# Performance work log

Hardware: AMD Instinct MI355X
Metric: run time of the kernel (lower is better)

Reference implementation:

```python
import jax, jax.numpy as jnp
import numpy as np

B, L, D = 4, 4096, 1024
K = D // 4

def setup_inputs() -> dict:
    key = jax.random.key(0)
    ks = jax.random.split(key, 16)
    def w(k, sh):
        return jax.random.normal(k, sh, dtype=jnp.float32) * 0.02
    return {
        'x': jax.random.normal(ks[0], (B, L, D), dtype=jnp.float32),
        'Wk1': w(ks[1], (D, D)), 'bk1': jnp.zeros((D,), jnp.float32),
        'Wk2': w(ks[2], (D, K * 4)), 'bk2': jnp.zeros((K * 4,), jnp.float32),
        'Wq1': w(ks[3], (D, D)), 'bq1': jnp.zeros((D,), jnp.float32),
        'Wq2': w(ks[4], (D, K * 4)), 'bq2': jnp.zeros((K * 4,), jnp.float32),
        'Wv': w(ks[5], (D, D)), 'bv': jnp.zeros((D,), jnp.float32),
        'gamma': jnp.ones((D,), jnp.float32), 'beta': jnp.zeros((D,), jnp.float32),
        'Wo': w(ks[6], (D, D)), 'bo': jnp.zeros((D,), jnp.float32),
    }

def _normalize(q, eps=1e-12):
    n = jnp.sqrt(jnp.sum(q * q, axis=-1, keepdims=True))
    return q / jnp.maximum(n, eps)

def _quat_conj(q):
    return q * jnp.asarray([1., -1., -1., -1.], dtype=q.dtype)

def _quat_mul(q1, q2):
    w1, x1, y1, z1 = q1[..., 0], q1[..., 1], q1[..., 2], q1[..., 3]
    w2, x2, y2, z2 = q2[..., 0], q2[..., 1], q2[..., 2], q2[..., 3]
    w = w1 * w2 - x1 * x2 - y1 * y2 - z1 * z2
    x = w1 * x2 + x1 * w2 + y1 * z2 - z1 * y2
    y = w1 * y2 - x1 * z2 + y1 * w2 + z1 * x2
    z = w1 * z2 + x1 * y2 - y1 * x2 + z1 * w2
    return jnp.stack([w, x, y, z], axis=-1)

def _quat_rotate(q, v):
    return _quat_mul(_quat_mul(q, v), _quat_conj(q))

def _mlp(x, W1, b1, W2, b2):
    h = jax.nn.gelu(x @ W1 + b1, approximate=False)
    return h @ W2 + b2

def _layernorm(x, g, b, eps=1e-5):
    mu = jnp.mean(x, axis=-1, keepdims=True)
    var = jnp.var(x, axis=-1, keepdims=True)
    return (x - mu) * jax.lax.rsqrt(var + eps) * g + b

def reference(x, Wk1, bk1, Wk2, bk2, Wq1, bq1, Wq2, bq2, Wv, bv, gamma, beta, Wo, bo):
    b, l, d = x.shape
    k = d // 4
    key_q = _normalize(_mlp(x, Wk1, bk1, Wk2, bk2).reshape(b, l, k, 4))
    query_q = _normalize(_mlp(x, Wq1, bq1, Wq2, bq2).reshape(b, l, k, 4))
    value = (x @ Wv + bv).reshape(b, l, k, 4)
    rotated = _quat_rotate(key_q, value)            # [B,L,K,4]
    memory = jnp.cumsum(rotated, axis=1)            # prefix-sum memory
    retrieved = _quat_rotate(_quat_conj(query_q), memory).reshape(b, l, d)
    norm = jnp.sqrt(jnp.arange(1, l + 1, dtype=x.dtype)).reshape(1, l, 1)
    out = _layernorm(retrieved / norm, gamma, beta) @ Wo + bo
    return x + out
```

## Files before the change

### kernel.cpp

```cpp
#include <hip/hip_runtime.h>
#include <cstddef>
#include <cstdint>

static constexpr int Bb  = 4;
static constexpr int Ll  = 4096;
static constexpr int Dd  = 1024;
static constexpr int Mm  = 16384;
static constexpr int KK  = 1024;
static constexpr int NTK = 32;

typedef __attribute__((ext_vector_type(8))) short short8;
typedef __attribute__((ext_vector_type(4))) float f32x4;

#define AS1C(p) ((const __attribute__((address_space(1))) void*)(p))
#define AS3(p)  ((__attribute__((address_space(3))) void*)(p))

__device__ __forceinline__ float b2f(unsigned short u) {
    union { unsigned int i; float f; } c; c.i = ((unsigned int)u) << 16; return c.f;
}
__device__ __forceinline__ unsigned short f2b(float f) {
    union { float f; unsigned int i; } c; c.f = f;
    unsigned int r = c.i + 0x7fffu + ((c.i >> 16) & 1u);
    return (unsigned short)(r >> 16);
}
__device__ __forceinline__ float4 qmul(const float4 a, const float4 b) {
    float4 r;
    r.x = a.x * b.x - a.y * b.y - a.z * b.z - a.w * b.w;
    r.y = a.x * b.y + a.y * b.x + a.z * b.w - a.w * b.z;
    r.z = a.x * b.z - a.y * b.w + a.z * b.x + a.w * b.y;
    r.w = a.x * b.w + a.y * b.z - a.z * b.y + a.w * b.x;
    return r;
}
__device__ __forceinline__ float4 qconj(const float4 a) {
    return make_float4(a.x, -a.y, -a.z, -a.w);
}
__device__ __forceinline__ float4 qnorm(const float4 a) {
    float n = sqrtf(a.x * a.x + a.y * a.y + a.z * a.z + a.w * a.w);
    float inv = 1.0f / fmaxf(n, 1e-12f);
    return make_float4(a.x * inv, a.y * inv, a.z * inv, a.w * inv);
}
__device__ __forceinline__ float gelu_fast(float v) {
    const float a = fabsf(v) * 0.70710678118654752f;
    const float t = 1.0f / (1.0f + 0.3275911f * a);
    const float p = t * (0.254829592f + t * (-0.284496736f + t * (1.421413741f
                   + t * (-1.453152027f + t * 1.061405429f))));
    const float e = __expf(-a * a);
    const float erfa = 1.0f - p * e;
    const float erfv = copysignf(erfa, v);
    return 0.5f * v * (1.0f + erfv);
}

__global__ __launch_bounds__(256)
void conv_k(const float* __restrict__ src, unsigned short* __restrict__ dst, int n4)
{
    const int i = blockIdx.x * 256 + threadIdx.x;
    if (i >= n4) return;
    const float4 v = reinterpret_cast<const float4*>(src)[i];
    ushort4 o;
    o.x = f2b(v.x); o.y = f2b(v.y); o.z = f2b(v.z); o.w = f2b(v.w);
    reinterpret_cast<ushort4*>(dst)[i] = o;
}

__global__ __launch_bounds__(256)
void wtrans_k(const float* __restrict__ src, unsigned short* __restrict__ dst)
{
    __shared__ float t[32][33];
    const int tx = threadIdx.x, ty = threadIdx.y;
    const int n0 = blockIdx.x * 32, k0 = blockIdx.y * 32;
    #pragma unroll
    for (int j = ty; j < 32; j += 8)
        t[j][tx] = src[(size_t)(k0 + j) * Dd + n0 + tx];
    __syncthreads();
    #pragma unroll
    for (int j = ty; j < 32; j += 8)
        dst[(size_t)(n0 + j) * Dd + k0 + tx] = f2b(t[tx][j]);
}

__global__ __launch_bounds__(256)
void bcat_k(const float* __restrict__ bk1, const float* __restrict__ bq1,
            const float* __restrict__ bv,  const float* __restrict__ bk2,
            const float* __restrict__ bq2, float* __restrict__ b1,
            float* __restrict__ b2)
{
    const int i = blockIdx.x * 256 + threadIdx.x;
    if (i < 3072) b1[i] = (i < 1024) ? bk1[i] : (i < 2048 ? bq1[i - 1024] : bv[i - 2048]);
    if (i < 2048) b2[i] = (i < 1024) ? bk2[i] : bq2[i - 1024];
}

template<int MODE>
__global__ __launch_bounds__(512, 2)
void gemm256_k(const unsigned short* __restrict__ A, int astride,
               const unsigned short* __restrict__ BT,
               const float* __restrict__ bias,
               const float* __restrict__ resid,
               unsigned short* __restrict__ outH,
               float* __restrict__ outF,
               int Nn)
{
    extern __shared__ char smem[];
    const int tid  = threadIdx.x;
    const int lane = tid & 63;
    const int w    = tid >> 6;
    const int wr   = w >> 2;
    const int wc   = w & 3;

    const int nwg = gridDim.x;
    const int cpx = nwg >> 3;
    const int bid = blockIdx.x;
    const int swz = (bid & 7) * cpx + (bid >> 3);
    const int nTN = Nn >> 8;
    const int m0  = (swz / nTN) << 8;
    const int n0  = (swz % nTN) << 8;
    const int aoff = (MODE == 1 && n0 >= 1024) ? 1024 : 0;

    const unsigned short* gA[2];
    const unsigned short* gB[2];
    #pragma unroll
    for (int c = 0; c < 2; ++c) {
        const int n16 = c * 512 + tid;
        const int line = n16 >> 3;
        const int u = (n16 & 7) ^ (line & 7);
        const int r = 2 * line + (u >> 2);
        const int kcs = u & 3;
        gA[c] = A + (size_t)(m0 + r) * astride + aoff + kcs * 8;
        gB[c] = BT + (size_t)(n0 + r) * KK + kcs * 8;
    }
    const int wslot = w * 1024;

    auto STAGE = [&](int kt, int bi) {
        const int koff = kt * 32;
        #pragma unroll
        for (int c = 0; c < 2; ++c) {
            __builtin_amdgcn_global_load_lds(AS1C(gA[c] + koff),
                AS3(smem + bi * 16384 + c * 8192 + wslot), 16, 0, 0);
            __builtin_amdgcn_global_load_lds(AS1C(gB[c] + koff),
                AS3(smem + 49152 + bi * 16384 + c * 8192 + wslot), 16, 0, 0);
        }
    };

    const int kc = lane >> 4;
    const int rl = lane & 15;
    int offA[8], offB[4];
    #pragma unroll
    for (int mi = 0; mi < 8; ++mi) {
        const int r = wr * 128 + mi * 16 + rl;
        offA[mi] = (r >> 1) * 128 + (((((r & 1) << 2) | kc) ^ ((r >> 1) & 7)) << 4);
    }
    #pragma unroll
    for (int ni = 0; ni < 4; ++ni) {
        const int r = wc * 64 + ni * 16 + rl;
        offB[ni] = 49152 + (r >> 1) * 128 + (((((r & 1) << 2) | kc) ^ ((r >> 1) & 7)) << 4);
    }

    f32x4 acc[8][4] = {};

    auto BODY = [&](int kt, int bi, int bi2, int vm, bool dostage) {
        if (dostage) STAGE(kt + 2, bi2);
        const char* Ab = smem + bi * 16384;
        short8 af[4], bf[4];
        #pragma unroll
        for (int ni = 0; ni < 4; ++ni) bf[ni] = *(const short8*)(smem + bi * 16384 + offB[ni]);
        #pragma unroll
        for (int mi = 0; mi < 4; ++mi) af[mi] = *(const short8*)(Ab + offA[mi]);
        __builtin_amdgcn_s_barrier();
        __builtin_amdgcn_s_setprio(1);
        #pragma unroll
        for (int mi = 0; mi < 4; ++mi)
            #pragma unroll
            for (int ni = 0; ni < 4; ++ni)
                acc[mi][ni] = __builtin_amdgcn_mfma_f32_16x16x32_bf16(af[mi], bf[ni], acc[mi][ni], 0, 0, 0);
        __builtin_amdgcn_s_setprio(0);
        __builtin_amdgcn_s_barrier();
        #pragma unroll
        for (int mi = 0; mi < 4; ++mi) af[mi] = *(const short8*)(Ab + offA[4 + mi]);
        __builtin_amdgcn_s_setprio(1);
        #pragma unroll
        for (int mi = 0; mi < 4; ++mi)
            #pragma unroll
            for (int ni = 0; ni < 4; ++ni)
                acc[4 + mi][ni] = __builtin_amdgcn_mfma_f32_16x16x32_bf16(af[mi], bf[ni], acc[4 + mi][ni], 0, 0, 0);
        __builtin_amdgcn_s_setprio(0);
        if (vm == 4)      asm volatile("s_waitcnt vmcnt(4)" ::: "memory");
        else if (vm == 0) asm volatile("s_waitcnt vmcnt(0)" ::: "memory");
        if (vm >= 0) __builtin_amdgcn_s_barrier();
    };

    STAGE(0, 0);
    STAGE(1, 1);
    asm volatile("s_waitcnt vmcnt(4)" ::: "memory");
    __builtin_amdgcn_s_barrier();

    for (int t0 = 0; t0 < NTK - 2; t0 += 3) {
        BODY(t0 + 0, 0, 2, 4, true);
        BODY(t0 + 1, 1, 0, 4, true);
        BODY(t0 + 2, 2, 1, 4, true);
    }
    BODY(NTK - 2, 0, 0, 0, false);
    BODY(NTK - 1, 1, 0, -1, false);

    const int colb = n0 + wc * 64 + rl;
    const int rowb = m0 + wr * 128 + kc * 4;
    #pragma unroll
    for (int ni = 0; ni < 4; ++ni) {
        const int col = colb + ni * 16;
        const float bv = bias[col];
        #pragma unroll
        for (int mi = 0; mi < 8; ++mi) {
            const int row0 = rowb + mi * 16;
            #pragma unroll
            for (int rr = 0; rr < 4; ++rr) {
                float v = acc[mi][ni][rr] + bv;
                const int row = row0 + rr;
                if (MODE == 0) {
                    if (n0 < 2048) outH[(size_t)row * 2048 + col] = f2b(gelu_fast(v));
                    else           outF[(size_t)row * 1024 + (col - 2048)] = v;
                } else if (MODE == 1) {
                    outH[(size_t)row * 2048 + col] = f2b(v);
                } else {
                    const size_t ix = (size_t)row * 1024 + col;
                    outF[ix] = v + resid[ix];
                }
            }
        }
    }
}

__global__ __launch_bounds__(256)
void rotfuse_k(const unsigned short* __restrict__ qb2, float* __restrict__ val,
               float* __restrict__ part)
{
    const int idx = blockIdx.x * 256 + threadIdx.x;
    const int kq  = idx & 255;
    const int ch  = (idx >> 8) & 63;
    const int b   = idx >> 14;
    const int row0 = b * Ll + ch * 64;
    float4 s = make_float4(0.f, 0.f, 0.f, 0.f);
    for (int i = 0; i < 64; ++i) {
        const int row = row0 + i;
        const ushort4 qu = *reinterpret_cast<const ushort4*>(qb2 + (size_t)row * 2048 + kq * 4);
        const float4 q = qnorm(make_float4(b2f(qu.x), b2f(qu.y), b2f(qu.z), b2f(qu.w)));
        float4* vp = reinterpret_cast<float4*>(val + (size_t)row * 1024 + kq * 4);
        const float4 r = qmul(qmul(q, *vp), qconj(q));
        *vp = r;
        s.x += r.x; s.y += r.y; s.z += r.z; s.w += r.w;
    }
    *reinterpret_cast<float4*>(part + (size_t)idx * 4) = s;
}

__global__ __launch_bounds__(256)
void scan2_k(float* __restrict__ part)
{
    const int idx = blockIdx.x * 256 + threadIdx.x;
    const int kq = idx & 255, b = idx >> 8;
    float4 run = make_float4(0.f, 0.f, 0.f, 0.f);
    for (int c = 0; c < 64; ++c) {
        float4* p = reinterpret_cast<float4*>(part + (((size_t)(b * 64 + c)) * 256 + kq) * 4);
        const float4 t = *p;
        *p = run;
        run.x += t.x; run.y += t.y; run.z += t.z; run.w += t.w;
    }
}

__global__ __launch_bounds__(256)
void scan3_k(float* __restrict__ val, const float* __restrict__ part)
{
    const int idx = blockIdx.x * 256 + threadIdx.x;
    const int kq  = idx & 255;
    const int ch  = (idx >> 8) & 63;
    const int b   = idx >> 14;
    const int row0 = b * Ll + ch * 64;
    float4 run = *reinterpret_cast<const float4*>(part + (size_t)idx * 4);
    for (int i = 0; i < 64; ++i) {
        float4* vp = reinterpret_cast<float4*>(val + (size_t)(row0 + i) * 1024 + kq * 4);
        const float4 v = *vp;
        run.x += v.x; run.y += v.y; run.z += v.z; run.w += v.w;
        *vp = run;
    }
}

__global__ __launch_bounds__(256)
void retrieve_ln_k(const float* __restrict__ mem, const unsigned short* __restrict__ qb2,
                   const float* __restrict__ gamma, const float* __restrict__ beta,
                   unsigned short* __restrict__ out)
{
    const int row = blockIdx.x;
    const int l   = row & (Ll - 1);
    const int t   = threadIdx.x;
    const size_t base = (size_t)row * 1024 + t * 4;

    const ushort4 qu = *reinterpret_cast<const ushort4*>(qb2 + (size_t)row * 2048 + 1024 + t * 4);
    const float4 q = qnorm(make_float4(b2f(qu.x), b2f(qu.y), b2f(qu.z), b2f(qu.w)));
    const float4 m4 = *reinterpret_cast<const float4*>(mem + base);
    float4 r = qmul(qmul(qconj(q), m4), q);

    const float inv = 1.0f / sqrtf((float)(l + 1));
    r.x *= inv; r.y *= inv; r.z *= inv; r.w *= inv;

    float s  = r.x + r.y + r.z + r.w;
    float ss = r.x * r.x + r.y * r.y + r.z * r.z + r.w * r.w;
    #pragma unroll
    for (int off = 32; off > 0; off >>= 1) {
        s  += __shfl_xor(s, off);
        ss += __shfl_xor(ss, off);
    }
    __shared__ float red[2][4];
    const int wid = t >> 6, lane = t & 63;
    if (lane == 0) { red[0][wid] = s; red[1][wid] = ss; }
    __syncthreads();
    const float sum = red[0][0] + red[0][1] + red[0][2] + red[0][3];
    const float ssq = red[1][0] + red[1][1] + red[1][2] + red[1][3];
    const float mu  = sum * (1.0f / 1024.0f);
    const float var = ssq * (1.0f / 1024.0f) - mu * mu;
    const float sc  = rsqrtf(var + 1e-5f);

    const float4 g4 = *reinterpret_cast<const float4*>(gamma + t * 4);
    const float4 b4 = *reinterpret_cast<const float4*>(beta  + t * 4);
    ushort4 o;
    o.x = f2b((r.x - mu) * sc * g4.x + b4.x);
    o.y = f2b((r.y - mu) * sc * g4.y + b4.y);
    o.z = f2b((r.z - mu) * sc * g4.z + b4.z);
    o.w = f2b((r.w - mu) * sc * g4.w + b4.w);
    *reinterpret_cast<ushort4*>(out + base) = o;
}

extern "C" void kernel_launch(void* const* d_in, const int* in_sizes, int n_in,
                              void* d_out, int out_size, void* d_ws, size_t ws_size,
                              hipStream_t stream)
{
    const float* x     = (const float*)d_in[0];
    const float* Wk1   = (const float*)d_in[1];
    const float* bk1   = (const float*)d_in[2];
    const float* Wk2   = (const float*)d_in[3];
    const float* bk2   = (const float*)d_in[4];
    const float* Wq1   = (const float*)d_in[5];
    const float* bq1   = (const float*)d_in[6];
    const float* Wq2   = (const float*)d_in[7];
    const float* bq2   = (const float*)d_in[8];
    const float* Wv    = (const float*)d_in[9];
    const float* bv    = (const float*)d_in[10];
    const float* gamma = (const float*)d_in[11];
    const float* beta  = (const float*)d_in[12];
    const float* Wo    = (const float*)d_in[13];
    const float* bo    = (const float*)d_in[14];
    float* out = (float*)d_out;

    const size_t TD = (size_t)Mm * 1024;
    const size_t DD = (size_t)1024 * 1024;

    unsigned short* qb2   = (unsigned short*)d_ws;
    unsigned short* xb    = qb2;
    unsigned short* wcat1 = qb2 + TD;
    unsigned short* h     = qb2 + 2 * TD;
    float*          bufB  = (float*)(h + 2 * TD);
    unsigned short* wcat2 = (unsigned short*)(bufB + TD);
    unsigned short* woT   = wcat2 + 2 * DD;
    float*          bcat1 = (float*)(woT + DD);
    float*          bcat2 = bcat1 + 3072;
    float*          part  = bcat2 + 2048;

    const dim3 blk(256);
    const dim3 tblk(32, 8);
    const dim3 tgrid(32, 32);

    (void)hipFuncSetAttribute((const void*)gemm256_k<0>, hipFuncAttributeMaxDynamicSharedMemorySize, 98304);
    (void)hipFuncSetAttribute((const void*)gemm256_k<1>, hipFuncAttributeMaxDynamicSharedMemorySize, 98304);
    (void)hipFuncSetAttribute((const void*)gemm256_k<2>, hipFuncAttributeMaxDynamicSharedMemorySize, 98304);

    conv_k<<<(int)(TD / 4 / 256), blk, 0, stream>>>(x, xb, (int)(TD / 4));
    wtrans_k<<<tgrid, tblk, 0, stream>>>(Wk1, wcat1);
    wtrans_k<<<tgrid, tblk, 0, stream>>>(Wq1, wcat1 + DD);
    wtrans_k<<<tgrid, tblk, 0, stream>>>(Wv,  wcat1 + 2 * DD);
    wtrans_k<<<tgrid, tblk, 0, stream>>>(Wk2, wcat2);
    wtrans_k<<<tgrid, tblk, 0, stream>>>(Wq2, wcat2 + DD);
    wtrans_k<<<tgrid, tblk, 0, stream>>>(Wo,  woT);
    bcat_k<<<12, blk, 0, stream>>>(bk1, bq1, bv, bk2, bq2, bcat1, bcat2);

    gemm256_k<0><<<64 * 12, 512, 98304, stream>>>(xb, 1024, wcat1, bcat1, nullptr, h, bufB, 3072);
    gemm256_k<1><<<64 * 8, 512, 98304, stream>>>(h, 2048, wcat2, bcat2, nullptr, qb2, nullptr, 2048);

    rotfuse_k<<<256, blk, 0, stream>>>(qb2, bufB, part);
    scan2_k<<<4, blk, 0, stream>>>(part);
    scan3_k<<<256, blk, 0, stream>>>(bufB, part);

    retrieve_ln_k<<<Mm, blk, 0, stream>>>(bufB, qb2, gamma, beta, h);

    gemm256_k<2><<<64 * 4, 512, 98304, stream>>>(h, 1024, woT, bo, x, nullptr, out, 1024);
}
```

Measured before the change: 464.5 us.

## Restructure GEMM main loop into double-buffered 64-wide k phases; stage bf16 epilogue through LDS

The bf16 GEMM now uses two 64-deep k buffers (128 KB of LDS) instead of three 32-deep buffers. Each k-step is split into four phases, and each phase issues one unit of the next tile's global-to-LDS loads between its MFMA groups, so copies are interleaved more finely with compute. The bf16-output epilogues (GELU hidden and the second MLP) now write into LDS first, then store to global with 16-byte row-contiguous vector stores instead of scattered 2-byte stores. The cost is more LDS per block and extra barriers in the epilogue.

```diff
diff --git a/kernel.cpp b/kernel.cpp
--- a/kernel.cpp
+++ b/kernel.cpp
@@ -4,10 +4,9 @@
 
 static constexpr int Bb  = 4;
 static constexpr int Ll  = 4096;
-static constexpr int Dd  = 1024;
 static constexpr int Mm  = 16384;
 static constexpr int KK  = 1024;
-static constexpr int NTK = 32;
+static constexpr int NT2 = 16;
 
 typedef __attribute__((ext_vector_type(8))) short short8;
 typedef __attribute__((ext_vector_type(4))) float f32x4;
@@ -46,8 +45,7 @@
                    + t * (-1.453152027f + t * 1.061405429f))));
     const float e = __expf(-a * a);
     const float erfa = 1.0f - p * e;
-    const float erfv = copysignf(erfa, v);
-    return 0.5f * v * (1.0f + erfv);
+    return 0.5f * v * (1.0f + copysignf(erfa, v));
 }
 
 __global__ __launch_bounds__(256)
@@ -69,11 +67,11 @@
     const int n0 = blockIdx.x * 32, k0 = blockIdx.y * 32;
     #pragma unroll
     for (int j = ty; j < 32; j += 8)
-        t[j][tx] = src[(size_t)(k0 + j) * Dd + n0 + tx];
+        t[j][tx] = src[(size_t)(k0 + j) * 1024 + n0 + tx];
     __syncthreads();
     #pragma unroll
     for (int j = ty; j < 32; j += 8)
-        dst[(size_t)(n0 + j) * Dd + k0 + tx] = f2b(t[tx][j]);
+        dst[(size_t)(n0 + j) * 1024 + k0 + tx] = f2b(t[tx][j]);
 }
 
 __global__ __launch_bounds__(256)
@@ -113,28 +111,27 @@
     const int n0  = (swz % nTN) << 8;
     const int aoff = (MODE == 1 && n0 >= 1024) ? 1024 : 0;
 
-    const unsigned short* gA[2];
-    const unsigned short* gB[2];
-    #pragma unroll
-    for (int c = 0; c < 2; ++c) {
-        const int n16 = c * 512 + tid;
-        const int line = n16 >> 3;
-        const int u = (n16 & 7) ^ (line & 7);
-        const int r = 2 * line + (u >> 2);
-        const int kcs = u & 3;
-        gA[c] = A + (size_t)(m0 + r) * astride + aoff + kcs * 8;
-        gB[c] = BT + (size_t)(n0 + r) * KK + kcs * 8;
-    }
-    const int wslot = w * 1024;
-
-    auto STAGE = [&](int kt, int bi) {
-        const int koff = kt * 32;
+    const unsigned short* pA[2];
+    const unsigned short* pB[2];
+    #pragma unroll
+    for (int c2 = 0; c2 < 2; ++c2) {
+        const int s = c2 * 512 + tid;
+        const int line = s >> 3;
+        const int v = (s & 7) ^ (line & 7);
+        const int r = 2 * line + (v >> 2);
+        const int kcs = v & 3;
+        pA[c2] = A + (size_t)(m0 + r) * astride + aoff + kcs * 8;
+        pB[c2] = BT + (size_t)(n0 + r) * KK + kcs * 8;
+    }
+
+    auto STAGE_UNIT = [&](int cdst, int matB, int khs, int t1) {
+        const int ks = t1 * 64 + khs * 32;
         #pragma unroll
-        for (int c = 0; c < 2; ++c) {
-            __builtin_amdgcn_global_load_lds(AS1C(gA[c] + koff),
-                AS3(smem + bi * 16384 + c * 8192 + wslot), 16, 0, 0);
-            __builtin_amdgcn_global_load_lds(AS1C(gB[c] + koff),
-                AS3(smem + 49152 + bi * 16384 + c * 8192 + wslot), 16, 0, 0);
+        for (int c2 = 0; c2 < 2; ++c2) {
+            __builtin_amdgcn_global_load_lds(
+                AS1C((matB ? pB[c2] : pA[c2]) + ks),
+                AS3(smem + cdst * 65536 + matB * 32768 + khs * 16384 + c2 * 8192 + w * 1024),
+                16, 0, 0);
         }
     };
 
@@ -149,76 +146,105 @@
     #pragma unroll
     for (int ni = 0; ni < 4; ++ni) {
         const int r = wc * 64 + ni * 16 + rl;
-        offB[ni] = 49152 + (r >> 1) * 128 + (((((r & 1) << 2) | kc) ^ ((r >> 1) & 7)) << 4);
+        offB[ni] = 32768 + (r >> 1) * 128 + (((((r & 1) << 2) | kc) ^ ((r >> 1) & 7)) << 4);
     }
 
     f32x4 acc[8][4] = {};
-
-    auto BODY = [&](int kt, int bi, int bi2, int vm, bool dostage) {
-        if (dostage) STAGE(kt + 2, bi2);
-        const char* Ab = smem + bi * 16384;
-        short8 af[4], bf[4];
-        #pragma unroll
-        for (int ni = 0; ni < 4; ++ni) bf[ni] = *(const short8*)(smem + bi * 16384 + offB[ni]);
-        #pragma unroll
-        for (int mi = 0; mi < 4; ++mi) af[mi] = *(const short8*)(Ab + offA[mi]);
-        __builtin_amdgcn_s_barrier();
+    short8 af[8];
+
+    auto PHASE = [&](int c, int kh, int nh, int su, int t1, int vm) {
+        const int base = c * 65536 + kh * 16384;
+        if (nh == 0) {
+            #pragma unroll
+            for (int mi = 0; mi < 8; ++mi)
+                af[mi] = *(const short8*)(smem + base + offA[mi]);
+        }
+        const short8 b0 = *(const short8*)(smem + base + offB[2 * nh + 0]);
+        const short8 b1 = *(const short8*)(smem + base + offB[2 * nh + 1]);
+        if (su >= 0) STAGE_UNIT(c ^ 1, su & 1, su >> 1, t1);
         __builtin_amdgcn_s_setprio(1);
         #pragma unroll
-        for (int mi = 0; mi < 4; ++mi)
-            #pragma unroll
-            for (int ni = 0; ni < 4; ++ni)
-                acc[mi][ni] = __builtin_amdgcn_mfma_f32_16x16x32_bf16(af[mi], bf[ni], acc[mi][ni], 0, 0, 0);
-        __builtin_amdgcn_s_setprio(0);
-        __builtin_amdgcn_s_barrier();
-        #pragma unroll
-        for (int mi = 0; mi < 4; ++mi) af[mi] = *(const short8*)(Ab + offA[4 + mi]);
-        __builtin_amdgcn_s_setprio(1);
-        #pragma unroll
-        for (int mi = 0; mi < 4; ++mi)
-            #pragma unroll
-            for (int ni = 0; ni < 4; ++ni)
-                acc[4 + mi][ni] = __builtin_amdgcn_mfma_f32_16x16x32_bf16(af[mi], bf[ni], acc[4 + mi][ni], 0, 0, 0);
+        for (int mi = 0; mi < 8; ++mi) {
+            acc[mi][2 * nh + 0] = __builtin_amdgcn_mfma_f32_16x16x32_bf16(af[mi], b0, acc[mi][2 * nh + 0], 0, 0, 0);
+            acc[mi][2 * nh + 1] = __builtin_amdgcn_mfma_f32_16x16x32_bf16(af[mi], b1, acc[mi][2 * nh + 1], 0, 0, 0);
+        }
         __builtin_amdgcn_s_setprio(0);
         if (vm == 4)      asm volatile("s_waitcnt vmcnt(4)" ::: "memory");
         else if (vm == 0) asm volatile("s_waitcnt vmcnt(0)" ::: "memory");
-        if (vm >= 0) __builtin_amdgcn_s_barrier();
+        if (vm >= -1) __builtin_amdgcn_s_barrier();
     };
 
-    STAGE(0, 0);
-    STAGE(1, 1);
-    asm volatile("s_waitcnt vmcnt(4)" ::: "memory");
+    STAGE_UNIT(0, 0, 0, 0);
+    STAGE_UNIT(0, 1, 0, 0);
+    STAGE_UNIT(0, 0, 1, 0);
+    STAGE_UNIT(0, 1, 1, 0);
+    asm volatile("s_waitcnt vmcnt(0)" ::: "memory");
     __builtin_amdgcn_s_barrier();
 
-    for (int t0 = 0; t0 < NTK - 2; t0 += 3) {
-        BODY(t0 + 0, 0, 2, 4, true);
-        BODY(t0 + 1, 1, 0, 4, true);
-        BODY(t0 + 2, 2, 1, 4, true);
-    }
-    BODY(NTK - 2, 0, 0, 0, false);
-    BODY(NTK - 1, 1, 0, -1, false);
+    for (int t = 0; t < NT2 - 1; ++t) {
+        const int c = t & 1;
+        PHASE(c, 0, 0, 0, t + 1, 4);
+        PHASE(c, 0, 1, 1, t + 1, 4);
+        PHASE(c, 1, 0, 2, t + 1, 4);
+        PHASE(c, 1, 1, 3, t + 1, 4);
+    }
+    PHASE(1, 0, 0, -1, 0, -1);
+    PHASE(1, 0, 1, -1, 0, 0);
+    PHASE(1, 1, 0, -1, 0, -2);
+    PHASE(1, 1, 1, -1, 0, -2);
+    __syncthreads();
 
     const int colb = n0 + wc * 64 + rl;
     const int rowb = m0 + wr * 128 + kc * 4;
-    #pragma unroll
-    for (int ni = 0; ni < 4; ++ni) {
-        const int col = colb + ni * 16;
-        const float bv = bias[col];
+    float bv[4];
+    #pragma unroll
+    for (int ni = 0; ni < 4; ++ni) bv[ni] = bias[colb + ni * 16];
+
+    const bool bf16out = (MODE == 1) || (MODE == 0 && n0 < 2048);
+    if (bf16out) {
+        unsigned short* eb = (unsigned short*)smem;
+        const int er = tid >> 2, eq = tid & 3;
         #pragma unroll
-        for (int mi = 0; mi < 8; ++mi) {
-            const int row0 = rowb + mi * 16;
+        for (int pass = 0; pass < 2; ++pass) {
+            if (wr == pass) {
+                #pragma unroll
+                for (int ni = 0; ni < 4; ++ni) {
+                    const int col = wc * 64 + ni * 16 + rl;
+                    #pragma unroll
+                    for (int mi = 0; mi < 8; ++mi)
+                        #pragma unroll
+                        for (int rr = 0; rr < 4; ++rr) {
+                            float v = acc[mi][ni][rr] + bv[ni];
+                            if (MODE == 0) v = gelu_fast(v);
+                            eb[(mi * 16 + kc * 4 + rr) * 264 + col] = f2b(v);
+                        }
+                }
+            }
+            __syncthreads();
+            const size_t grow = (size_t)(m0 + pass * 128 + er) * 2048 + n0 + eq * 64;
             #pragma unroll
-            for (int rr = 0; rr < 4; ++rr) {
-                float v = acc[mi][ni][rr] + bv;
-                const int row = row0 + rr;
-                if (MODE == 0) {
-                    if (n0 < 2048) outH[(size_t)row * 2048 + col] = f2b(gelu_fast(v));
-                    else           outF[(size_t)row * 1024 + (col - 2048)] = v;
-                } else if (MODE == 1) {
-                    outH[(size_t)row * 2048 + col] = f2b(v);
-                } else {
-                    const size_t ix = (size_t)row * 1024 + col;
-                    outF[ix] = v + resid[ix];
+            for (int j = 0; j < 8; ++j) {
+                *(uint4*)(outH + grow + j * 8) =
+                    *(const uint4*)(eb + er * 264 + eq * 64 + j * 8);
+            }
+            __syncthreads();
+        }
+    } else {
+        #pragma unroll
+        for (int ni = 0; ni < 4; ++ni) {
+            const int col = colb + ni * 16;
+            #pragma unroll
+            for (int mi = 0; mi < 8; ++mi) {
+                #pragma unroll
+                for (int rr = 0; rr < 4; ++rr) {
+                    float v = acc[mi][ni][rr] + bv[ni];
+                    const int row = rowb + mi * 16 + rr;
+                    if (MODE == 0) {
+                        outF[(size_t)row * 1024 + (col - 2048)] = v;
+                    } else {
+                        const size_t ix = (size_t)row * 1024 + col;
+                        outF[ix] = v + resid[ix];
+                    }
                 }
             }
         }
@@ -362,9 +388,9 @@
     const dim3 tblk(32, 8);
     const dim3 tgrid(32, 32);
 
-    (void)hipFuncSetAttribute((const void*)gemm256_k<0>, hipFuncAttributeMaxDynamicSharedMemorySize, 98304);
-    (void)hipFuncSetAttribute((const void*)gemm256_k<1>, hipFuncAttributeMaxDynamicSharedMemorySize, 98304);
-    (void)hipFuncSetAttribute((const void*)gemm256_k<2>, hipFuncAttributeMaxDynamicSharedMemorySize, 98304);
+    (void)hipFuncSetAttribute((const void*)gemm256_k<0>, hipFuncAttributeMaxDynamicSharedMemorySize, 131072);
+    (void)hipFuncSetAttribute((const void*)gemm256_k<1>, hipFuncAttributeMaxDynamicSharedMemorySize, 131072);
+    (void)hipFuncSetAttribute((const void*)gemm256_k<2>, hipFuncAttributeMaxDynamicSharedMemorySize, 131072);
 
     conv_k<<<(int)(TD / 4 / 256), blk, 0, stream>>>(x, xb, (int)(TD / 4));
     wtrans_k<<<tgrid, tblk, 0, stream>>>(Wk1, wcat1);
@@ -375,8 +401,8 @@
     wtrans_k<<<tgrid, tblk, 0, stream>>>(Wo,  woT);
     bcat_k<<<12, blk, 0, stream>>>(bk1, bq1, bv, bk2, bq2, bcat1, bcat2);
 
-    gemm256_k<0><<<64 * 12, 512, 98304, stream>>>(xb, 1024, wcat1, bcat1, nullptr, h, bufB, 3072);
-    gemm256_k<1><<<64 * 8, 512, 98304, stream>>>(h, 2048, wcat2, bcat2, nullptr, qb2, nullptr, 2048);
+    gemm256_k<0><<<64 * 12, 512, 131072, stream>>>(xb, 1024, wcat1, bcat1, nullptr, h, bufB, 3072);
+    gemm256_k<1><<<64 * 8, 512, 131072, stream>>>(h, 2048, wcat2, bcat2, nullptr, qb2, nullptr, 2048);
 
     rotfuse_k<<<256, blk, 0, stream>>>(qb2, bufB, part);
     scan2_k<<<4, blk, 0, stream>>>(part);
@@ -384,5 +410,5 @@
 
     retrieve_ln_k<<<Mm, blk, 0, stream>>>(bufB, qb2, gamma, beta, h);
 
-    gemm256_k<2><<<64 * 4, 512, 98304, stream>>>(h, 1024, woT, bo, x, nullptr, out, 1024);
-}
+    gemm256_k<2><<<64 * 4, 512, 131072, stream>>>(h, 1024, woT, bo, x, nullptr, out, 1024);
+}
```

Result: slower. 480.6 us (+3.5%).
